# Kernel tuning notes

Measured on AMD Instinct MI355X. Metric: run time of the kernel, lower is better.

## Reference

```python
import jax, jax.numpy as jnp
import numpy as np

B, N, DIM = 2, 2048, 1024
H, DH = 16, 64
INNER = H * DH  # 1024
SCALE = DH ** -0.5
EPS = 1e-5


def setup_inputs() -> dict:
    key = jax.random.key(0)
    ks = jax.random.split(key, 7)
    s = 0.02
    return {
        "x": jax.random.normal(ks[0], (B, N, DIM), dtype=jnp.float32),
        "ln_gamma": jnp.ones((DIM,), jnp.float32),
        "ln_beta": jnp.zeros((DIM,), jnp.float32),
        "W_qkv": jax.random.normal(ks[1], (DIM, 3 * INNER), jnp.float32) * s,
        "b_qkv": jnp.zeros((3 * INNER,), jnp.float32),
        "W_out": jax.random.normal(ks[2], (INNER, DIM), jnp.float32) * s,
        "b_out": jnp.zeros((DIM,), jnp.float32),
    }


def reference(x, ln_gamma, ln_beta, W_qkv, b_qkv, W_out, b_out):
    # LayerNorm over last dim
    mu = jnp.mean(x, axis=-1, keepdims=True)
    var = jnp.mean(jnp.square(x - mu), axis=-1, keepdims=True)
    xn = (x - mu) * jax.lax.rsqrt(var + EPS) * ln_gamma + ln_beta
    # QKV projection
    qkv = xn @ W_qkv + b_qkv                      # [b, n, 3*inner]
    q, k, v = jnp.split(qkv, 3, axis=-1)
    # [b, n, (h d)] -> [b, h, n, d]
    to_heads = lambda t: t.reshape(B, N, H, DH).transpose(0, 2, 1, 3)
    q, k, v = to_heads(q), to_heads(k), to_heads(v)
    # naive attention (explicit score matrix, matching the original)
    qk = jnp.einsum('bhnd,bhmd->bhnm', q, k) * SCALE
    attn = jax.nn.softmax(qk, axis=-1)
    out = jnp.einsum('bhnm,bhmd->bhnd', attn, v)  # [b, h, n, d]
    out = out.transpose(0, 2, 1, 3).reshape(B, N, INNER)
    return out @ W_out + b_out
```

## Files before the change

### kernel.cpp

```cpp
#include <hip/hip_runtime.h>

typedef unsigned short u16;
typedef unsigned int   u32;
typedef __attribute__((ext_vector_type(2)))  unsigned u32x2;
typedef __attribute__((ext_vector_type(4)))  float  f32x4;
typedef __attribute__((ext_vector_type(8)))  short  s16x8;

__device__ __forceinline__ u16 f2bf(float f) {
  unsigned u = __builtin_bit_cast(unsigned, f);
  u += 0x7FFFu + ((u >> 16) & 1u);
  return (u16)(u >> 16);
}

__device__ __forceinline__ float exp2g(float x) { return __builtin_amdgcn_exp2f(x); }

__device__ __forceinline__ void gload16(const void* g, void* l) {
  __builtin_amdgcn_global_load_lds(
      (const __attribute__((address_space(1))) void*)g,
      (__attribute__((address_space(3))) void*)l, 16, 0, 0);
}

__global__ __launch_bounds__(256) void ln_kernel(
    const float* __restrict__ x, const float* __restrict__ gamma,
    const float* __restrict__ beta, u16* __restrict__ xn)
{
  const int row = blockIdx.x, tid = threadIdx.x;
  const float* xr = x + (size_t)row * 1024;
  float4 v = *(const float4*)(xr + tid * 4);
  float s  = v.x + v.y + v.z + v.w;
  float s2 = v.x*v.x + v.y*v.y + v.z*v.z + v.w*v.w;
#pragma unroll
  for (int off = 32; off >= 1; off >>= 1) {
    s  += __shfl_xor(s,  off);
    s2 += __shfl_xor(s2, off);
  }
  __shared__ float red[8];
  const int w = tid >> 6, l = tid & 63;
  if (l == 0) { red[w] = s; red[w + 4] = s2; }
  __syncthreads();
  s  = red[0] + red[1] + red[2] + red[3];
  s2 = red[4] + red[5] + red[6] + red[7];
  const float mu  = s * (1.0f / 1024.0f);
  const float var = s2 * (1.0f / 1024.0f) - mu * mu;
  const float rs  = rsqrtf(var + 1e-5f);
  float4 g  = *(const float4*)(gamma + tid * 4);
  float4 be = *(const float4*)(beta  + tid * 4);
  ushort4 o;
  o.x = f2bf((v.x - mu) * rs * g.x + be.x);
  o.y = f2bf((v.y - mu) * rs * g.y + be.y);
  o.z = f2bf((v.z - mu) * rs * g.z + be.z);
  o.w = f2bf((v.w - mu) * rs * g.w + be.w);
  *(ushort4*)(xn + (size_t)row * 1024 + tid * 4) = o;
}

__global__ void transpose_cvt(const float* __restrict__ in, u16* __restrict__ out,
                              int R, int C)
{
  __shared__ float t[32][33];
  const int bc = blockIdx.x * 32, br = blockIdx.y * 32;
  const int x = threadIdx.x;
#pragma unroll
  for (int i = threadIdx.y; i < 32; i += 8)
    t[i][x] = in[(size_t)(br + i) * C + bc + x];
  __syncthreads();
#pragma unroll
  for (int i = threadIdx.y; i < 32; i += 8)
    out[(size_t)(bc + i) * R + br + x] = f2bf(t[x][i]);
}

__device__ __forceinline__ void store_out(float* p, float v) { *p = v; }
__device__ __forceinline__ void store_out(u16* p, float v)   { *p = f2bf(v); }

template <typename OutT>
__global__ __launch_bounds__(256) void gemm_bt(
    const u16* __restrict__ A, const u16* __restrict__ Bt,
    const float* __restrict__ bias, OutT* __restrict__ C,
    int M, int N, int K)
{
  __shared__ u16 As[2][128 * 32];
  __shared__ u16 Bs[2][128 * 32];
  const int tid = threadIdx.x;
  const int w = tid >> 6, l = tid & 63;
  const int g = l >> 4, li = l & 15;
  const int bm = blockIdx.y * 128, bn = blockIdx.x * 128;
  const int wr = (w >> 1) * 64, wc = (w & 1) * 64;

  f32x4 acc[4][4] = {};

  const int ar0 = tid >> 2,          as0 = tid & 3;
  const int ar1 = (tid + 256) >> 2,  as1 = (tid + 256) & 3;
  const u16* pa0 = A  + (size_t)(bm + ar0) * K + 8 * (as0 ^ (ar0 & 3));
  const u16* pa1 = A  + (size_t)(bm + ar1) * K + 8 * (as1 ^ (ar1 & 3));
  const u16* pb0 = Bt + (size_t)(bn + ar0) * K + 8 * (as0 ^ (ar0 & 3));
  const u16* pb1 = Bt + (size_t)(bn + ar1) * K + 8 * (as1 ^ (ar1 & 3));

  auto stage = [&](int b, int kt) {
    gload16(pa0 + kt, &As[b][w * 512]);
    gload16(pa1 + kt, &As[b][2048 + w * 512]);
    gload16(pb0 + kt, &Bs[b][w * 512]);
    gload16(pb1 + kt, &Bs[b][2048 + w * 512]);
  };

  stage(0, 0);
  if (K > 32) stage(1, 32);

  int buf = 0;
  for (int kt = 0; kt < K; kt += 32) {
    if (kt + 32 < K) asm volatile("s_waitcnt vmcnt(4)" ::: "memory");
    else             asm volatile("s_waitcnt vmcnt(0)" ::: "memory");
    __builtin_amdgcn_s_barrier();

    const u16* as = &As[buf][0];
    const u16* bs = &Bs[buf][0];

    s16x8 af[4], bf[4];
#pragma unroll
    for (int m = 0; m < 4; ++m) {
      const int row = wr + m * 16 + li;
      af[m] = *(const s16x8*)(as + row * 32 + 8 * (g ^ (row & 3)));
    }
#pragma unroll
    for (int n = 0; n < 4; ++n) {
      const int row = wc + n * 16 + li;
      bf[n] = *(const s16x8*)(bs + row * 32 + 8 * (g ^ (row & 3)));
    }
    __builtin_amdgcn_s_setprio(1);
#pragma unroll
    for (int m = 0; m < 4; ++m)
#pragma unroll
      for (int n = 0; n < 4; ++n)
        acc[m][n] = __builtin_amdgcn_mfma_f32_16x16x32_bf16(af[m], bf[n], acc[m][n], 0, 0, 0);
    __builtin_amdgcn_s_setprio(0);

    __builtin_amdgcn_s_barrier();
    if (kt + 64 < K) stage(buf, kt + 64);
    buf ^= 1;
  }

#pragma unroll
  for (int n = 0; n < 4; ++n) {
    const int col = bn + wc + n * 16 + li;
    const float bv = bias[col];
#pragma unroll
    for (int m = 0; m < 4; ++m) {
      const int row0 = bm + wr + m * 16 + g * 4;
#pragma unroll
      for (int r = 0; r < 4; ++r)
        store_out(C + (size_t)(row0 + r) * N + col, acc[m][n][r] + bv);
    }
  }
}

template <typename OutT>
__global__ __launch_bounds__(256) void gemm_bt64(
    const u16* __restrict__ A, const u16* __restrict__ Bt,
    const float* __restrict__ bias, OutT* __restrict__ C,
    int M, int N, int K)
{
  __shared__ u16 As[2][64 * 32];
  __shared__ u16 Bs[2][128 * 32];
  const int tid = threadIdx.x;
  const int w = tid >> 6, l = tid & 63;
  const int g = l >> 4, li = l & 15;
  const int bm = blockIdx.y * 64, bn = blockIdx.x * 128;
  const int wr = (w >> 1) * 32, wc = (w & 1) * 64;

  f32x4 acc[2][4] = {};

  const int ar = tid >> 2,           asl = tid & 3;
  const int br0 = tid >> 2,          bs0 = tid & 3;
  const int br1 = (tid + 256) >> 2,  bs1 = (tid + 256) & 3;
  const u16* pa  = A  + (size_t)(bm + ar)  * K + 8 * (asl ^ (ar  & 3));
  const u16* pb0 = Bt + (size_t)(bn + br0) * K + 8 * (bs0 ^ (br0 & 3));
  const u16* pb1 = Bt + (size_t)(bn + br1) * K + 8 * (bs1 ^ (br1 & 3));

  auto stage = [&](int b, int kt) {
    gload16(pa  + kt, &As[b][w * 512]);
    gload16(pb0 + kt, &Bs[b][w * 512]);
    gload16(pb1 + kt, &Bs[b][2048 + w * 512]);
  };

  stage(0, 0);
  if (K > 32) stage(1, 32);

  int buf = 0;
  for (int kt = 0; kt < K; kt += 32) {
    if (kt + 32 < K) asm volatile("s_waitcnt vmcnt(3)" ::: "memory");
    else             asm volatile("s_waitcnt vmcnt(0)" ::: "memory");
    __builtin_amdgcn_s_barrier();

    const u16* as = &As[buf][0];
    const u16* bs = &Bs[buf][0];

    s16x8 af[2], bf[4];
#pragma unroll
    for (int m = 0; m < 2; ++m) {
      const int row = wr + m * 16 + li;
      af[m] = *(const s16x8*)(as + row * 32 + 8 * (g ^ (row & 3)));
    }
#pragma unroll
    for (int n = 0; n < 4; ++n) {
      const int row = wc + n * 16 + li;
      bf[n] = *(const s16x8*)(bs + row * 32 + 8 * (g ^ (row & 3)));
    }
    __builtin_amdgcn_s_setprio(1);
#pragma unroll
    for (int m = 0; m < 2; ++m)
#pragma unroll
      for (int n = 0; n < 4; ++n)
        acc[m][n] = __builtin_amdgcn_mfma_f32_16x16x32_bf16(af[m], bf[n], acc[m][n], 0, 0, 0);
    __builtin_amdgcn_s_setprio(0);

    __builtin_amdgcn_s_barrier();
    if (kt + 64 < K) stage(buf, kt + 64);
    buf ^= 1;
  }

#pragma unroll
  for (int n = 0; n < 4; ++n) {
    const int col = bn + wc + n * 16 + li;
    const float bv = bias[col];
#pragma unroll
    for (int m = 0; m < 2; ++m) {
      const int row0 = bm + wr + m * 16 + g * 4;
#pragma unroll
      for (int r = 0; r < 4; ++r)
        store_out(C + (size_t)(row0 + r) * N + col, acc[m][n][r] + bv);
    }
  }
}

__global__ __launch_bounds__(256, 4) void attn_kernel(
    const u16* __restrict__ qkv, u16* __restrict__ outp)
{
  __shared__ u16 Ks[2][4096];
  __shared__ u16 Vt[4096];
  __shared__ u16 Pl[4 * 1024];

  const int tid = threadIdx.x;
  const int w = tid >> 6, l = tid & 63;
  const int g = l >> 4, li = l & 15;

  const int lb = (blockIdx.x & 7) * 128 + (blockIdx.x >> 3);
  const int qt = lb & 31;
  const int h  = (lb >> 5) & 15;
  const int bb = lb >> 9;
  const size_t baserow = (size_t)bb * 2048;

  const int qbase = qt * 64 + w * 16;
  const u16* qp = qkv + (baserow + qbase + li) * 3072 + h * 64 + 8 * g;
  const s16x8 qf0 = *(const s16x8*)(qp);
  const s16x8 qf1 = *(const s16x8*)(qp + 32);

  const int kr0 = tid >> 3,         kc0 = tid & 7;
  const int kr1 = (tid + 256) >> 3, kc1 = (tid + 256) & 7;
  const u16* kg0 = qkv + (baserow + kr0) * 3072 + 1024 + h * 64 + 8 * (kc0 ^ (kr0 & 7));
  const u16* kg1 = qkv + (baserow + kr1) * 3072 + 1024 + h * 64 + 8 * (kc1 ^ (kr1 & 7));

  const int vp = tid >> 3, dg = tid & 7;
  const u16* vgA = qkv + (baserow + 2 * vp)     * 3072 + 2048 + h * 64 + 8 * dg;
  const u16* vgB = qkv + (baserow + 2 * vp + 1) * 3072 + 2048 + h * 64 + 8 * dg;

  auto issueK = [&](int b, int t) {
    const size_t koff = (size_t)t * (64 * 3072);
    gload16(kg0 + koff, &Ks[b][w * 512]);
    gload16(kg1 + koff, &Ks[b][2048 + w * 512]);
  };

  const float C1  = 0.18033688f;
  const float THR = 11.5416f;
  float M = -1e30f;
  f32x4 o[4] = {}, os = {};

  s16x8 ones;
#pragma unroll
  for (int j = 0; j < 8; ++j) ones[j] = (short)0x3F80;

  char* Pw = (char*)(Pl + w * 1024);
  const int pswz = (li & 7) << 4;

  issueK(0, 0);
  s16x8 va = *(const s16x8*)vgA;
  s16x8 vb = *(const s16x8*)vgB;

  int buf = 0;
  for (int t = 0; t < 32; ++t) {
#pragma unroll
    for (int j = 0; j < 8; ++j) {
      const int d = 8 * dg + j;
      const u32 val = (u32)(u16)va[j] | ((u32)(u16)vb[j] << 16);
      *(u32*)((char*)Vt + d * 128 + ((4 * vp) ^ ((((d ^ (d >> 3)) & 7)) << 4))) = val;
    }
    __syncthreads();

    if (t < 31) {
      issueK(buf ^ 1, t + 1);
      const size_t koff = (size_t)(t + 1) * (64 * 3072);
      va = *(const s16x8*)(vgA + koff);
      vb = *(const s16x8*)(vgB + koff);
    }

    const u16* kb = &Ks[buf][0];

    f32x4 s[4] = {};
    __builtin_amdgcn_s_setprio(1);
#pragma unroll
    for (int nk = 0; nk < 4; ++nk) {
      const int kvr = nk * 16 + li;
      const s16x8 kf0 = *(const s16x8*)((const char*)kb + kvr * 128 + 16 * ((0 + g) ^ (kvr & 7)));
      const s16x8 kf1 = *(const s16x8*)((const char*)kb + kvr * 128 + 16 * ((4 + g) ^ (kvr & 7)));
      s[nk] = __builtin_amdgcn_mfma_f32_16x16x32_bf16(kf0, qf0, s[nk], 0, 0, 0);
      s[nk] = __builtin_amdgcn_mfma_f32_16x16x32_bf16(kf1, qf1, s[nk], 0, 0, 0);
    }
    __builtin_amdgcn_s_setprio(0);

    float lm = fmaxf(fmaxf(s[0][0], s[0][1]), fmaxf(s[0][2], s[0][3]));
#pragma unroll
    for (int nk = 1; nk < 4; ++nk)
      lm = fmaxf(lm, fmaxf(fmaxf(s[nk][0], s[nk][1]), fmaxf(s[nk][2], s[nk][3])));
    lm = fmaxf(lm, __shfl_xor(lm, 16));
    lm = fmaxf(lm, __shfl_xor(lm, 32));
    lm *= C1;

    if (__any(lm > M + THR)) {
      const float mn = fmaxf(M, lm);
      const float a = exp2g(M - mn);
      M = mn;
      os[0] *= a;
#pragma unroll
      for (int nd = 0; nd < 4; ++nd)
#pragma unroll
        for (int r = 0; r < 4; ++r) o[nd][r] *= a;
    }

#pragma unroll
    for (int nk = 0; nk < 4; ++nk)
#pragma unroll
      for (int r = 0; r < 4; ++r)
        s[nk][r] = exp2g(fmaf(s[nk][r], C1, -M));

#pragma unroll
    for (int nk = 0; nk < 4; ++nk) {
      u32 lo, hi;
      asm("v_cvt_pk_bf16_f32 %0, %1, %2" : "=v"(lo) : "v"(s[nk][0]), "v"(s[nk][1]));
      asm("v_cvt_pk_bf16_f32 %0, %1, %2" : "=v"(hi) : "v"(s[nk][2]), "v"(s[nk][3]));
      *(u32x2*)(Pw + li * 128 + ((nk * 32 + 8 * g) ^ pswz)) = (u32x2){lo, hi};
    }
    asm volatile("s_waitcnt lgkmcnt(0)" ::: "memory");

    __builtin_amdgcn_s_setprio(1);
#pragma unroll
    for (int ks = 0; ks < 2; ++ks) {
      const s16x8 pf = *(const s16x8*)(Pw + li * 128 + ((ks * 64 + 16 * g) ^ pswz));
#pragma unroll
      for (int nd = 0; nd < 4; ++nd) {
        const int d = nd * 16 + li;
        const s16x8 vf = *(const s16x8*)((char*)Vt + d * 128 + ((ks * 64 + 16 * g) ^ (((d ^ (d >> 3)) & 7) << 4)));
        o[nd] = __builtin_amdgcn_mfma_f32_16x16x32_bf16(vf, pf, o[nd], 0, 0, 0);
      }
      os = __builtin_amdgcn_mfma_f32_16x16x32_bf16(ones, pf, os, 0, 0, 0);
    }
    __builtin_amdgcn_s_setprio(0);

    __syncthreads();
    buf ^= 1;
  }

  const float inv = 1.0f / os[0];
  const size_t row = baserow + qbase + li;
#pragma unroll
  for (int nd = 0; nd < 4; ++nd) {
    ushort4 st;
    st.x = f2bf(o[nd][0] * inv);
    st.y = f2bf(o[nd][1] * inv);
    st.z = f2bf(o[nd][2] * inv);
    st.w = f2bf(o[nd][3] * inv);
    *(ushort4*)(outp + row * 1024 + h * 64 + nd * 16 + 4 * g) = st;
  }
}

extern "C" void kernel_launch(void* const* d_in, const int* in_sizes, int n_in,
                              void* d_out, int out_size, void* d_ws, size_t ws_size,
                              hipStream_t stream)
{
  const float* x     = (const float*)d_in[0];
  const float* gamma = (const float*)d_in[1];
  const float* beta  = (const float*)d_in[2];
  const float* Wqkv  = (const float*)d_in[3];
  const float* bqkv  = (const float*)d_in[4];
  const float* Wout  = (const float*)d_in[5];
  const float* bout  = (const float*)d_in[6];
  float* out = (float*)d_out;

  char* ws = (char*)d_ws;
  u16* xn     = (u16*)(ws);
  u16* wqkv_t = (u16*)(ws + ((size_t)8  << 20));
  u16* wout_t = (u16*)(ws + ((size_t)14 << 20));
  u16* qkv    = (u16*)(ws + ((size_t)16 << 20));
  u16* attn   = (u16*)(ws + ((size_t)40 << 20));

  ln_kernel<<<4096, 256, 0, stream>>>(x, gamma, beta, xn);
  transpose_cvt<<<dim3(96, 32), dim3(32, 8), 0, stream>>>(Wqkv, wqkv_t, 1024, 3072);
  transpose_cvt<<<dim3(32, 32), dim3(32, 8), 0, stream>>>(Wout, wout_t, 1024, 1024);
  gemm_bt<u16><<<dim3(24, 32), 256, 0, stream>>>(xn, wqkv_t, bqkv, qkv, 4096, 3072, 1024);
  attn_kernel<<<1024, 256, 0, stream>>>(qkv, attn);
  gemm_bt64<float><<<dim3(8, 64), 256, 0, stream>>>(attn, wout_t, bout, out, 4096, 1024, 1024);
}
```

Before: 131.6 us.

## Process two 16-row query tiles per wave in attention to reuse K/V fragments

```diff
diff --git a/kernel.cpp b/kernel.cpp
--- a/kernel.cpp
+++ b/kernel.cpp
@@ -230,27 +230,30 @@
   }
 }
 
-__global__ __launch_bounds__(256, 4) void attn_kernel(
+__global__ __launch_bounds__(256, 2) void attn_kernel(
     const u16* __restrict__ qkv, u16* __restrict__ outp)
 {
   __shared__ u16 Ks[2][4096];
   __shared__ u16 Vt[4096];
-  __shared__ u16 Pl[4 * 1024];
+  __shared__ u16 Pl[4 * 2048];
 
   const int tid = threadIdx.x;
   const int w = tid >> 6, l = tid & 63;
   const int g = l >> 4, li = l & 15;
 
-  const int lb = (blockIdx.x & 7) * 128 + (blockIdx.x >> 3);
-  const int qt = lb & 31;
-  const int h  = (lb >> 5) & 15;
-  const int bb = lb >> 9;
+  const int lb = (blockIdx.x & 7) * 64 + (blockIdx.x >> 3);
+  const int qt = lb & 15;
+  const int h  = (lb >> 4) & 15;
+  const int bb = lb >> 8;
   const size_t baserow = (size_t)bb * 2048;
 
-  const int qbase = qt * 64 + w * 16;
-  const u16* qp = qkv + (baserow + qbase + li) * 3072 + h * 64 + 8 * g;
-  const s16x8 qf0 = *(const s16x8*)(qp);
-  const s16x8 qf1 = *(const s16x8*)(qp + 32);
+  const int qbase = qt * 128 + w * 32;
+  const u16* qpA = qkv + (baserow + qbase + li) * 3072 + h * 64 + 8 * g;
+  const u16* qpB = qpA + (size_t)16 * 3072;
+  const s16x8 qfA0 = *(const s16x8*)(qpA);
+  const s16x8 qfA1 = *(const s16x8*)(qpA + 32);
+  const s16x8 qfB0 = *(const s16x8*)(qpB);
+  const s16x8 qfB1 = *(const s16x8*)(qpB + 32);
 
   const int kr0 = tid >> 3,         kc0 = tid & 7;
   const int kr1 = (tid + 256) >> 3, kc1 = (tid + 256) & 7;
@@ -269,14 +272,15 @@
 
   const float C1  = 0.18033688f;
   const float THR = 11.5416f;
-  float M = -1e30f;
-  f32x4 o[4] = {}, os = {};
+  float MA = -1e30f, MB = -1e30f;
+  f32x4 oA[4] = {}, oB[4] = {}, osA = {}, osB = {};
 
   s16x8 ones;
 #pragma unroll
   for (int j = 0; j < 8; ++j) ones[j] = (short)0x3F80;
 
-  char* Pw = (char*)(Pl + w * 1024);
+  char* PwA = (char*)(Pl + w * 2048);
+  char* PwB = PwA + 2048;
   const int pswz = (li & 7) << 4;
 
   issueK(0, 0);
@@ -302,63 +306,88 @@
 
     const u16* kb = &Ks[buf][0];
 
-    f32x4 s[4] = {};
+    f32x4 sA[4] = {}, sB[4] = {};
     __builtin_amdgcn_s_setprio(1);
 #pragma unroll
     for (int nk = 0; nk < 4; ++nk) {
       const int kvr = nk * 16 + li;
       const s16x8 kf0 = *(const s16x8*)((const char*)kb + kvr * 128 + 16 * ((0 + g) ^ (kvr & 7)));
       const s16x8 kf1 = *(const s16x8*)((const char*)kb + kvr * 128 + 16 * ((4 + g) ^ (kvr & 7)));
-      s[nk] = __builtin_amdgcn_mfma_f32_16x16x32_bf16(kf0, qf0, s[nk], 0, 0, 0);
-      s[nk] = __builtin_amdgcn_mfma_f32_16x16x32_bf16(kf1, qf1, s[nk], 0, 0, 0);
+      sA[nk] = __builtin_amdgcn_mfma_f32_16x16x32_bf16(kf0, qfA0, sA[nk], 0, 0, 0);
+      sA[nk] = __builtin_amdgcn_mfma_f32_16x16x32_bf16(kf1, qfA1, sA[nk], 0, 0, 0);
+      sB[nk] = __builtin_amdgcn_mfma_f32_16x16x32_bf16(kf0, qfB0, sB[nk], 0, 0, 0);
+      sB[nk] = __builtin_amdgcn_mfma_f32_16x16x32_bf16(kf1, qfB1, sB[nk], 0, 0, 0);
     }
     __builtin_amdgcn_s_setprio(0);
 
-    float lm = fmaxf(fmaxf(s[0][0], s[0][1]), fmaxf(s[0][2], s[0][3]));
-#pragma unroll
-    for (int nk = 1; nk < 4; ++nk)
-      lm = fmaxf(lm, fmaxf(fmaxf(s[nk][0], s[nk][1]), fmaxf(s[nk][2], s[nk][3])));
-    lm = fmaxf(lm, __shfl_xor(lm, 16));
-    lm = fmaxf(lm, __shfl_xor(lm, 32));
-    lm *= C1;
-
-    if (__any(lm > M + THR)) {
-      const float mn = fmaxf(M, lm);
-      const float a = exp2g(M - mn);
-      M = mn;
-      os[0] *= a;
+    float lmA = fmaxf(fmaxf(sA[0][0], sA[0][1]), fmaxf(sA[0][2], sA[0][3]));
+    float lmB = fmaxf(fmaxf(sB[0][0], sB[0][1]), fmaxf(sB[0][2], sB[0][3]));
+#pragma unroll
+    for (int nk = 1; nk < 4; ++nk) {
+      lmA = fmaxf(lmA, fmaxf(fmaxf(sA[nk][0], sA[nk][1]), fmaxf(sA[nk][2], sA[nk][3])));
+      lmB = fmaxf(lmB, fmaxf(fmaxf(sB[nk][0], sB[nk][1]), fmaxf(sB[nk][2], sB[nk][3])));
+    }
+    lmA = fmaxf(lmA, __shfl_xor(lmA, 16));
+    lmA = fmaxf(lmA, __shfl_xor(lmA, 32));
+    lmB = fmaxf(lmB, __shfl_xor(lmB, 16));
+    lmB = fmaxf(lmB, __shfl_xor(lmB, 32));
+    lmA *= C1;
+    lmB *= C1;
+
+    if (__any((lmA > MA + THR) | (lmB > MB + THR))) {
+      const float mnA = fmaxf(MA, lmA);
+      const float mnB = fmaxf(MB, lmB);
+      const float aA = exp2g(MA - mnA);
+      const float aB = exp2g(MB - mnB);
+      MA = mnA; MB = mnB;
+      osA[0] *= aA; osB[0] *= aB;
 #pragma unroll
       for (int nd = 0; nd < 4; ++nd)
 #pragma unroll
-        for (int r = 0; r < 4; ++r) o[nd][r] *= a;
+        for (int r = 0; r < 4; ++r) { oA[nd][r] *= aA; oB[nd][r] *= aB; }
     }
 
 #pragma unroll
     for (int nk = 0; nk < 4; ++nk)
 #pragma unroll
-      for (int r = 0; r < 4; ++r)
-        s[nk][r] = exp2g(fmaf(s[nk][r], C1, -M));
+      for (int r = 0; r < 4; ++r) {
+        sA[nk][r] = exp2g(fmaf(sA[nk][r], C1, -MA));
+        sB[nk][r] = exp2g(fmaf(sB[nk][r], C1, -MB));
+      }
 
 #pragma unroll
     for (int nk = 0; nk < 4; ++nk) {
-      u32 lo, hi;
-      asm("v_cvt_pk_bf16_f32 %0, %1, %2" : "=v"(lo) : "v"(s[nk][0]), "v"(s[nk][1]));
-      asm("v_cvt_pk_bf16_f32 %0, %1, %2" : "=v"(hi) : "v"(s[nk][2]), "v"(s[nk][3]));
-      *(u32x2*)(Pw + li * 128 + ((nk * 32 + 8 * g) ^ pswz)) = (u32x2){lo, hi};
+      u32 loA, hiA, loB, hiB;
+      asm("v_cvt_pk_bf16_f32 %0, %1, %2" : "=v"(loA) : "v"(sA[nk][0]), "v"(sA[nk][1]));
+      asm("v_cvt_pk_bf16_f32 %0, %1, %2" : "=v"(hiA) : "v"(sA[nk][2]), "v"(sA[nk][3]));
+      asm("v_cvt_pk_bf16_f32 %0, %1, %2" : "=v"(loB) : "v"(sB[nk][0]), "v"(sB[nk][1]));
+      asm("v_cvt_pk_bf16_f32 %0, %1, %2" : "=v"(hiB) : "v"(sB[nk][2]), "v"(sB[nk][3]));
+      *(u32x2*)(PwA + li * 128 + ((nk * 32 + 8 * g) ^ pswz)) = (u32x2){loA, hiA};
+      *(u32x2*)(PwB + li * 128 + ((nk * 32 + 8 * g) ^ pswz)) = (u32x2){loB, hiB};
     }
     asm volatile("s_waitcnt lgkmcnt(0)" ::: "memory");
 
-    __builtin_amdgcn_s_setprio(1);
-#pragma unroll
-    for (int ks = 0; ks < 2; ++ks) {
-      const s16x8 pf = *(const s16x8*)(Pw + li * 128 + ((ks * 64 + 16 * g) ^ pswz));
+    s16x8 vf[2][4];
+#pragma unroll
+    for (int ks = 0; ks < 2; ++ks)
 #pragma unroll
       for (int nd = 0; nd < 4; ++nd) {
         const int d = nd * 16 + li;
-        const s16x8 vf = *(const s16x8*)((char*)Vt + d * 128 + ((ks * 64 + 16 * g) ^ (((d ^ (d >> 3)) & 7) << 4)));
-        o[nd] = __builtin_amdgcn_mfma_f32_16x16x32_bf16(vf, pf, o[nd], 0, 0, 0);
+        vf[ks][nd] = *(const s16x8*)((char*)Vt + d * 128 + ((ks * 64 + 16 * g) ^ (((d ^ (d >> 3)) & 7) << 4)));
       }
-      os = __builtin_amdgcn_mfma_f32_16x16x32_bf16(ones, pf, os, 0, 0, 0);
+
+    __builtin_amdgcn_s_setprio(1);
+#pragma unroll
+    for (int ks = 0; ks < 2; ++ks) {
+      const s16x8 pfA = *(const s16x8*)(PwA + li * 128 + ((ks * 64 + 16 * g) ^ pswz));
+      const s16x8 pfB = *(const s16x8*)(PwB + li * 128 + ((ks * 64 + 16 * g) ^ pswz));
+#pragma unroll
+      for (int nd = 0; nd < 4; ++nd) {
+        oA[nd] = __builtin_amdgcn_mfma_f32_16x16x32_bf16(vf[ks][nd], pfA, oA[nd], 0, 0, 0);
+        oB[nd] = __builtin_amdgcn_mfma_f32_16x16x32_bf16(vf[ks][nd], pfB, oB[nd], 0, 0, 0);
+      }
+      osA = __builtin_amdgcn_mfma_f32_16x16x32_bf16(ones, pfA, osA, 0, 0, 0);
+      osB = __builtin_amdgcn_mfma_f32_16x16x32_bf16(ones, pfB, osB, 0, 0, 0);
     }
     __builtin_amdgcn_s_setprio(0);
 
@@ -366,16 +395,22 @@
     buf ^= 1;
   }
 
-  const float inv = 1.0f / os[0];
-  const size_t row = baserow + qbase + li;
+  const float invA = 1.0f / osA[0];
+  const float invB = 1.0f / osB[0];
+  const size_t rowA = baserow + qbase + li;
 #pragma unroll
   for (int nd = 0; nd < 4; ++nd) {
-    ushort4 st;
-    st.x = f2bf(o[nd][0] * inv);
-    st.y = f2bf(o[nd][1] * inv);
-    st.z = f2bf(o[nd][2] * inv);
-    st.w = f2bf(o[nd][3] * inv);
-    *(ushort4*)(outp + row * 1024 + h * 64 + nd * 16 + 4 * g) = st;
+    ushort4 stA, stB;
+    stA.x = f2bf(oA[nd][0] * invA);
+    stA.y = f2bf(oA[nd][1] * invA);
+    stA.z = f2bf(oA[nd][2] * invA);
+    stA.w = f2bf(oA[nd][3] * invA);
+    stB.x = f2bf(oB[nd][0] * invB);
+    stB.y = f2bf(oB[nd][1] * invB);
+    stB.z = f2bf(oB[nd][2] * invB);
+    stB.w = f2bf(oB[nd][3] * invB);
+    *(ushort4*)(outp + rowA * 1024 + h * 64 + nd * 16 + 4 * g)        = stA;
+    *(ushort4*)(outp + (rowA + 16) * 1024 + h * 64 + nd * 16 + 4 * g) = stB;
   }
 }
 
@@ -403,6 +438,6 @@
   transpose_cvt<<<dim3(96, 32), dim3(32, 8), 0, stream>>>(Wqkv, wqkv_t, 1024, 3072);
   transpose_cvt<<<dim3(32, 32), dim3(32, 8), 0, stream>>>(Wout, wout_t, 1024, 1024);
   gemm_bt<u16><<<dim3(24, 32), 256, 0, stream>>>(xn, wqkv_t, bqkv, qkv, 4096, 3072, 1024);
-  attn_kernel<<<1024, 256, 0, stream>>>(qkv, attn);
+  attn_kernel<<<512, 256, 0, stream>>>(qkv, attn);
   gemm_bt64<float><<<dim3(8, 64), 256, 0, stream>>>(attn, wout_t, bout, out, 4096, 1024, 1024);
 }
```

New measurement: 131.8 us. About the same (+0.1%).
